# Optimization experiments

Measured on AMD Instinct MI355X. Metric: run time of the kernel, lower is better.

## Reference

```python
import jax, jax.numpy as jnp
import numpy as np

DIM = 64
N_GRAPHS = 300
N_NODES = 12000
N_EDGES = 40000


def setup_inputs() -> dict:
    key = jax.random.key(0)
    ks = jax.random.split(key, 16)
    N, E, F_IN, D = N_NODES, N_EDGES, 14, DIM

    def w(k, shape, fan_in):
        return jax.random.normal(k, shape, dtype=jnp.float32) / np.float32(np.sqrt(fan_in))

    return {
        "x": jax.random.normal(ks[0], (N, F_IN), dtype=jnp.float32),
        "edge_index": jax.random.randint(ks[1], (2, E), 0, N),
        "edge_attr": jax.random.uniform(ks[2], (E, 4), dtype=jnp.float32),
        "batch": jnp.sort(jax.random.randint(ks[3], (N,), 0, N_GRAPHS)),
        # lin0
        "lin0_w": w(ks[4], (D, F_IN), F_IN), "lin0_b": jnp.zeros((D,), jnp.float32),
        # edge MLP: Linear(4,128) -> ReLU -> Linear(128, D*D)
        "nn1_w": w(ks[5], (128, 4), 4), "nn1_b": jnp.zeros((128,), jnp.float32),
        "nn2_w": w(ks[6], (D * D, 128), 128), "nn2_b": jnp.zeros((D * D,), jnp.float32),
        # NNConv root weight + bias
        "root_w": w(ks[7], (D, D), D), "conv_b": jnp.zeros((D,), jnp.float32),
        # GRU(D, D), gate order r,z,n
        "gru_w_ih": w(ks[8], (3 * D, D), D), "gru_w_hh": w(ks[9], (3 * D, D), D),
        "gru_b_ih": jnp.zeros((3 * D,), jnp.float32), "gru_b_hh": jnp.zeros((3 * D,), jnp.float32),
        # Set2Set LSTM(2D -> D), gate order i,f,g,o
        "lstm_w_ih": w(ks[10], (4 * D, 2 * D), 2 * D), "lstm_w_hh": w(ks[11], (4 * D, D), D),
        "lstm_b_ih": jnp.zeros((4 * D,), jnp.float32), "lstm_b_hh": jnp.zeros((4 * D,), jnp.float32),
        # readout
        "lin1_w": w(ks[12], (D, 2 * D), 2 * D), "lin1_b": jnp.zeros((D,), jnp.float32),
        "lin2_w": w(ks[13], (1, D), D), "lin2_b": jnp.zeros((1,), jnp.float32),
    }


def _mpnn_forward(x, edge_index, edge_attr, batch,
                  lin0_w, lin0_b, nn1_w, nn1_b, nn2_w, nn2_b, root_w, conv_b,
                  gru_w_ih, gru_w_hh, gru_b_ih, gru_b_hh,
                  lstm_w_ih, lstm_w_hh, lstm_b_ih, lstm_b_hh,
                  lin1_w, lin1_b, lin2_w, lin2_b):
    N, D, B = x.shape[0], DIM, N_GRAPHS
    src, dst = edge_index[0], edge_index[1]

    out = jax.nn.relu(x @ lin0_w.T + lin0_b)          # [N, D]
    h = out

    # per-edge weight matrices from edge MLP: [E, D, D]
    W_e = (jax.nn.relu(edge_attr @ nn1_w.T + nn1_b) @ nn2_w.T + nn2_b).reshape(-1, D, D)
    deg = jnp.maximum(
        jax.ops.segment_sum(jnp.ones(src.shape, x.dtype), dst, num_segments=N), 1.0)

    for _ in range(3):
        # NNConv: gather -> per-edge bmm -> scatter-mean, plus root term and bias
        msg = jnp.einsum('ei,eio->eo', out[src], W_e)                 # [E, D]
        agg = jax.ops.segment_sum(msg, dst, num_segments=N) / deg[:, None]
        m = jax.nn.relu(out @ root_w + agg + conv_b)
        # GRU cell (torch gate order r, z, n)
        gx = m @ gru_w_ih.T + gru_b_ih
        gh = h @ gru_w_hh.T + gru_b_hh
        r = jax.nn.sigmoid(gx[:, :D] + gh[:, :D])
        z = jax.nn.sigmoid(gx[:, D:2 * D] + gh[:, D:2 * D])
        n = jnp.tanh(gx[:, 2 * D:] + r * gh[:, 2 * D:])
        h = (1.0 - z) * n + z * h
        out = h

    per_atom_out = out

    # Set2Set pooling, 3 processing steps
    q_star = jnp.zeros((B, 2 * D), x.dtype)
    hs = jnp.zeros((B, D), x.dtype)
    cs = jnp.zeros((B, D), x.dtype)
    for _ in range(3):
        gates = q_star @ lstm_w_ih.T + lstm_b_ih + hs @ lstm_w_hh.T + lstm_b_hh
        i_g = jax.nn.sigmoid(gates[:, 0 * D:1 * D])
        f_g = jax.nn.sigmoid(gates[:, 1 * D:2 * D])
        g_g = jnp.tanh(gates[:, 2 * D:3 * D])
        o_g = jax.nn.sigmoid(gates[:, 3 * D:4 * D])
        cs = f_g * cs + i_g * g_g
        hs = o_g * jnp.tanh(cs)
        q = hs                                                         # [B, D]
        e = jnp.sum(out * q[batch], axis=-1)                           # [N]
        e_max = jax.ops.segment_max(e, batch, num_segments=B)
        a = jnp.exp(e - e_max[batch])
        a = a / jax.ops.segment_sum(a, batch, num_segments=B)[batch]   # scatter-softmax
        r_read = jax.ops.segment_sum(a[:, None] * out, batch, num_segments=B)
        q_star = jnp.concatenate([q, r_read], axis=-1)                 # [B, 2D]

    y = jax.nn.relu(q_star @ lin1_w.T + lin1_b)
    y = (y @ lin2_w.T + lin2_b).reshape(-1)                            # [B]
    return (y, per_atom_out)


def reference(x, edge_index, edge_attr, batch,
              lin0_w, lin0_b, nn1_w, nn1_b, nn2_w, nn2_b, root_w, conv_b,
              gru_w_ih, gru_w_hh, gru_b_ih, gru_b_hh,
              lstm_w_ih, lstm_w_hh, lstm_b_ih, lstm_b_hh,
              lin1_w, lin1_b, lin2_w, lin2_b):
    return _mpnn_forward(x, edge_index, edge_attr, batch,
                         lin0_w, lin0_b, nn1_w, nn1_b, nn2_w, nn2_b, root_w, conv_b,
                         gru_w_ih, gru_w_hh, gru_b_ih, gru_b_hh,
                         lstm_w_ih, lstm_w_hh, lstm_b_ih, lstm_b_hh,
                         lin1_w, lin1_b, lin2_w, lin2_b)
```

## Files before the change

### kernel.cpp

```cpp
#include <hip/hip_runtime.h>
#include <math.h>

#define NBG 300
#define KP 8256

typedef __attribute__((ext_vector_type(8))) short short8_t;
typedef __attribute__((ext_vector_type(4))) float f32x4_t;

#define MFMA16(a,b,c) __builtin_amdgcn_mfma_f32_16x16x32_bf16(a,b,c,0,0,0)

__device__ __forceinline__ float sigmoidf_(float x){ return 1.0f/(1.0f+expf(-x)); }
__device__ __forceinline__ float bf2f(short s){
  union{unsigned u; float f;} v; v.u = ((unsigned)(unsigned short)s) << 16; return v.f;
}
__device__ __forceinline__ short f2bf(float f){
  union{float f; unsigned u;} v; v.f = f;
  unsigned r = (v.u + 0x7fffu + ((v.u >> 16) & 1u)) >> 16;
  return (short)r;
}
__device__ __forceinline__ unsigned cvt_pk_bf16(float lo, float hi){
  unsigned r;
  asm volatile("v_cvt_pk_bf16_f32 %0, %1, %2" : "=v"(r) : "v"(lo), "v"(hi));
  return r;
}
union FragA { short8_t v; unsigned u[4]; };

__device__ __forceinline__ short8_t frag_from(float sv, short8_t h){
  union { short8_t v; unsigned u[4]; } hh; hh.v = h;
  FragA fa;
  #pragma unroll
  for (int k2 = 0; k2 < 4; ++k2){
    float lo = __uint_as_float(hh.u[k2] << 16);
    float hi = __uint_as_float(hh.u[k2] & 0xffff0000u);
    fa.u[k2] = cvt_pk_bf16(sv*lo, sv*hi);
  }
  return fa.v;
}

__global__ void lin0_kernel(const float* __restrict__ x, const float* __restrict__ w,
                            const float* __restrict__ b, float* __restrict__ out,
                            short* __restrict__ out_bf, int N){
  int n = blockIdx.x; int d = threadIdx.x;
  __shared__ float xs[16];
  if (d < 14) xs[d] = x[n*14 + d];
  __syncthreads();
  float acc = b[d];
  #pragma unroll
  for (int k = 0; k < 14; ++k) acc = fmaf(xs[k], w[d*14 + k], acc);
  float v = fmaxf(acc, 0.0f);
  out[n*64 + d] = v;
  out_bf[n*64 + d] = f2bf(v);
}

__global__ void ehid_kernel(const float* __restrict__ ea, const float* __restrict__ w,
                            const float* __restrict__ b, short* __restrict__ hid_bf, int E){
  int e = blockIdx.x; int t = threadIdx.x;
  __shared__ float as[4];
  if (t < 4) as[t] = ea[e*4 + t];
  __syncthreads();
  float acc = b[t];
  #pragma unroll
  for (int k = 0; k < 4; ++k) acc = fmaf(as[k], w[t*4 + k], acc);
  hid_bf[(size_t)e*128 + t] = f2bf(fmaxf(acc, 0.0f));
}

__global__ void count2_kernel(const int* __restrict__ dstv, int E,
                              const int* __restrict__ batch, int N,
                              int* __restrict__ counts, int* __restrict__ bcounts){
  int i = blockIdx.x*blockDim.x + threadIdx.x;
  if (i < E) atomicAdd(&counts[dstv[i]], 1);
  int j = i - E;
  if (j >= 0 && j < N) atomicAdd(&bcounts[batch[j]], 1);
}

__global__ __launch_bounds__(1024) void scan2_kernel(
    const int* __restrict__ countsA, int* __restrict__ startsA, int* __restrict__ cursorA, int NA,
    const int* __restrict__ countsB, int* __restrict__ startsB, int* __restrict__ cursorB, int NB){
  const int* counts = blockIdx.x ? countsB : countsA;
  int* starts = blockIdx.x ? startsB : startsA;
  int* cursor = blockIdx.x ? cursorB : cursorA;
  int N = blockIdx.x ? NB : NA;
  __shared__ int part[1024];
  int t = threadIdx.x;
  int per = (N + 1023) >> 10;
  int base = t * per;
  int s = 0;
  for (int j = 0; j < per; ++j){ int idx = base + j; if (idx < N) s += counts[idx]; }
  part[t] = s;
  __syncthreads();
  for (int off = 1; off < 1024; off <<= 1){
    int v = (t >= off) ? part[t - off] : 0;
    __syncthreads();
    part[t] += v;
    __syncthreads();
  }
  int run = (t == 0) ? 0 : part[t-1];
  for (int j = 0; j < per; ++j){
    int idx = base + j;
    if (idx < N){ starts[idx] = run; cursor[idx] = run; run += counts[idx]; }
  }
}

__global__ void scatter_kernel(const int* __restrict__ dst, int* __restrict__ cursor,
                               int* __restrict__ sorted_eid, int E){
  int e = blockIdx.x*blockDim.x + threadIdx.x;
  if (e < E){ int p = atomicAdd(&cursor[dst[e]], 1); sorted_eid[p] = e; }
}

__global__ void w2t_build(const float* __restrict__ w2, const float* __restrict__ b2,
                          short* __restrict__ W2t){
  int o = blockIdx.x;
  for (int k = threadIdx.x; k < KP; k += blockDim.x){
    float val;
    if (k < 8192){ int i = k >> 7, h = k & 127; val = w2[(size_t)(i*64 + o)*128 + h]; }
    else val = b2[(k - 8192)*64 + o];
    W2t[(size_t)o*KP + k] = f2bf(val);
  }
}

__global__ __launch_bounds__(256) void msg_gemm3(
    const short* __restrict__ out_bf, const short* __restrict__ hid_bf,
    const short* __restrict__ W2t, const int* __restrict__ sorted,
    const int* __restrict__ src, const int* __restrict__ dstv,
    float* __restrict__ agg, int E)
{
  __shared__ short sSb[128*80];
  __shared__ __align__(16) char bufB[4][4096];
  __shared__ int eid_s[128];
  __shared__ int dst_s[128];

  const int tid = threadIdx.x;
  const int blk = blockIdx.x;
  const int split = blockIdx.y;

  if (tid < 128){
    int p = blk*128 + tid;
    int e = (p < E) ? sorted[p] : -1;
    eid_s[tid] = e;
    dst_s[tid] = (e >= 0) ? dstv[e] : -1;
  }
  __syncthreads();

  const int lane = tid & 63, wid = tid >> 6;
  const int r = lane & 15, q4 = lane >> 4;
  const int eloc0 = wid*32 + r;
  const int eloc1 = eloc0 + 16;

  short8_t z8 = {0,0,0,0,0,0,0,0};

  {
    int row = tid >> 1, half = tid & 1;
    int e = eid_s[row];
    short* dp = sSb + row*80 + half*32;
    if (e >= 0){
      const short* sp = out_bf + (size_t)src[e]*64 + half*32;
      *(short8_t*)(dp)      = *(const short8_t*)(sp);
      *(short8_t*)(dp + 8)  = *(const short8_t*)(sp + 8);
      *(short8_t*)(dp + 16) = *(const short8_t*)(sp + 16);
      *(short8_t*)(dp + 24) = *(const short8_t*)(sp + 24);
    } else {
      *(short8_t*)(dp) = z8; *(short8_t*)(dp + 8) = z8;
      *(short8_t*)(dp + 16) = z8; *(short8_t*)(dp + 24) = z8;
    }
  }

  short8_t hq0_0=z8, hq0_1=z8, hq0_2=z8, hq0_3=z8;
  short8_t hq1_0=z8, hq1_1=z8, hq1_2=z8, hq1_3=z8;
  {
    int e0 = eid_s[eloc0], e1 = eid_s[eloc1];
    if (e0 >= 0){
      const short* hp = hid_bf + (size_t)e0*128 + q4*8;
      hq0_0 = *(const short8_t*)(hp);      hq0_1 = *(const short8_t*)(hp + 32);
      hq0_2 = *(const short8_t*)(hp + 64); hq0_3 = *(const short8_t*)(hp + 96);
    }
    if (e1 >= 0){
      const short* hp = hid_bf + (size_t)e1*128 + q4*8;
      hq1_0 = *(const short8_t*)(hp);      hq1_1 = *(const short8_t*)(hp + 32);
      hq1_2 = *(const short8_t*)(hp + 64); hq1_3 = *(const short8_t*)(hp + 96);
    }
  }

  const int gl_o  = tid >> 2;
  const int gl_kq = (tid & 3) ^ ((tid >> 3) & 3);
  const char* w2b = (const char*)W2t;
  const size_t gbase = (size_t)gl_o*(KP*2) + (size_t)gl_kq*16;

  int boff0, boff1, boff2, boff3;
  {
    int o0 = r, o1 = 16 + r, o2 = 32 + r, o3 = 48 + r;
    boff0 = (o0*4 + (q4 ^ ((o0 >> 1) & 3))) * 16;
    boff1 = (o1*4 + (q4 ^ ((o1 >> 1) & 3))) * 16;
    boff2 = (o2*4 + (q4 ^ ((o2 >> 1) & 3))) * 16;
    boff3 = (o3*4 + (q4 ^ ((o3 >> 1) & 3))) * 16;
  }

  const bool last  = (split == 3);
  const int cstart = split * 64;
  const int nc     = last ? 66 : 64;
  const int clast  = cstart + nc - 1;

#define GLOAD(c_, bi_)                                                          \
  __builtin_amdgcn_global_load_lds(                                             \
      (const __attribute__((address_space(1))) unsigned*)(w2b + gbase + (size_t)(c_)*64), \
      (__attribute__((address_space(3))) unsigned*)(&bufB[bi_][wid*1024]), 16, 0, 0)

  GLOAD(cstart + 0, (cstart + 0) & 3);
  GLOAD(cstart + 1, (cstart + 1) & 3);
  GLOAD(cstart + 2, (cstart + 2) & 3);
  __syncthreads();

  f32x4_t zz = {0.f,0.f,0.f,0.f};
  f32x4_t acc00 = zz, acc01 = zz, acc02 = zz, acc03 = zz;
  f32x4_t acc10 = zz, acc11 = zz, acc12 = zz, acc13 = zz;

#define CHUNK(QI, Q, HQ0, HQ1)                                                  \
  {                                                                             \
    int c = cstart + (QI)*4 + (Q);                                              \
    asm volatile("s_waitcnt vmcnt(2) lgkmcnt(0)" ::: "memory");                 \
    __builtin_amdgcn_s_barrier();                                               \
    const char* bp = bufB[c & 3];                                               \
    short8_t b0 = *(const short8_t*)(bp + boff0);                               \
    short8_t b1 = *(const short8_t*)(bp + boff1);                               \
    short8_t b2 = *(const short8_t*)(bp + boff2);                               \
    short8_t b3 = *(const short8_t*)(bp + boff3);                               \
    { int cn = c + 3; if (cn > clast) cn = clast; GLOAD(cn, (c + 3) & 3); }     \
    short8_t f0 = frag_from(sv0, HQ0);                                          \
    short8_t f1 = frag_from(sv1, HQ1);                                          \
    acc00 = MFMA16(f0, b0, acc00);                                              \
    acc01 = MFMA16(f0, b1, acc01);                                              \
    acc02 = MFMA16(f0, b2, acc02);                                              \
    acc03 = MFMA16(f0, b3, acc03);                                              \
    acc10 = MFMA16(f1, b0, acc10);                                              \
    acc11 = MFMA16(f1, b1, acc11);                                              \
    acc12 = MFMA16(f1, b2, acc12);                                              \
    acc13 = MFMA16(f1, b3, acc13);                                              \
  }

  #pragma unroll 1
  for (int qi = 0; qi < 16; ++qi){
    int qg = (split << 4) + qi;
    float sv0 = bf2f(sSb[eloc0*80 + qg]);
    float sv1 = bf2f(sSb[eloc1*80 + qg]);
    CHUNK(qi, 0, hq0_0, hq1_0)
    CHUNK(qi, 1, hq0_1, hq1_1)
    CHUNK(qi, 2, hq0_2, hq1_2)
    CHUNK(qi, 3, hq0_3, hq1_3)
  }

  if (last){
    #pragma unroll 1
    for (int tc = 0; tc < 2; ++tc){
      int c = 256 + tc;
      asm volatile("s_waitcnt vmcnt(2) lgkmcnt(0)" ::: "memory");
      __builtin_amdgcn_s_barrier();
      const char* bp = bufB[c & 3];
      short8_t b0 = *(const short8_t*)(bp + boff0);
      short8_t b1 = *(const short8_t*)(bp + boff1);
      short8_t b2 = *(const short8_t*)(bp + boff2);
      short8_t b3 = *(const short8_t*)(bp + boff3);
      GLOAD(clast, (c + 3) & 3);
      short8_t f0 = *(const short8_t*)(sSb + eloc0*80 + tc*32 + q4*8);
      short8_t f1 = *(const short8_t*)(sSb + eloc1*80 + tc*32 + q4*8);
      acc00 = MFMA16(f0, b0, acc00);
      acc01 = MFMA16(f0, b1, acc01);
      acc02 = MFMA16(f0, b2, acc02);
      acc03 = MFMA16(f0, b3, acc03);
      acc10 = MFMA16(f1, b0, acc10);
      acc11 = MFMA16(f1, b1, acc11);
      acc12 = MFMA16(f1, b2, acc12);
      acc13 = MFMA16(f1, b3, acc13);
    }
  }

  asm volatile("s_waitcnt vmcnt(0)" ::: "memory");

  {
    int ebase = wid*32 + q4*4;
    float c0 = 0.f, c1 = 0.f, c2 = 0.f, c3 = 0.f;
    #pragma unroll
    for (int reg = 0; reg < 4; ++reg){
      c0 += acc00[reg]; c1 += acc01[reg]; c2 += acc02[reg]; c3 += acc03[reg];
      int d = dst_s[ebase + reg];
      int dn = (reg < 3) ? dst_s[ebase + reg + 1] : -2;
      if (d != dn){
        if (d >= 0){
          float* ap = agg + (size_t)d*64;
          atomicAdd(ap + r,      c0);
          atomicAdd(ap + 16 + r, c1);
          atomicAdd(ap + 32 + r, c2);
          atomicAdd(ap + 48 + r, c3);
        }
        c0 = c1 = c2 = c3 = 0.f;
      }
    }
  }
  {
    int ebase = wid*32 + 16 + q4*4;
    float c0 = 0.f, c1 = 0.f, c2 = 0.f, c3 = 0.f;
    #pragma unroll
    for (int reg = 0; reg < 4; ++reg){
      c0 += acc10[reg]; c1 += acc11[reg]; c2 += acc12[reg]; c3 += acc13[reg];
      int d = dst_s[ebase + reg];
      int dn = (reg < 3) ? dst_s[ebase + reg + 1] : -2;
      if (d != dn){
        if (d >= 0){
          float* ap = agg + (size_t)d*64;
          atomicAdd(ap + r,      c0);
          atomicAdd(ap + 16 + r, c1);
          atomicAdd(ap + 32 + r, c2);
          atomicAdd(ap + 48 + r, c3);
        }
        c0 = c1 = c2 = c3 = 0.f;
      }
    }
  }
#undef CHUNK
#undef GLOAD
}

__global__ __launch_bounds__(256) void node_mfma(
    const short* __restrict__ out_bf, float* __restrict__ agg,
    const int* __restrict__ counts,
    const float* __restrict__ root_w, const float* __restrict__ conv_b,
    const float* __restrict__ gwih, const float* __restrict__ gwhh,
    const float* __restrict__ gbih, const float* __restrict__ gbhh,
    float* __restrict__ out, short* __restrict__ out_bf_w,
    float* __restrict__ out_dup, int N)
{
  __shared__ short XH[64*128];
  __shared__ short rootT[64*64];
  __shared__ short Wih_s[192*64];
  __shared__ short Whh_s[192*64];
  __shared__ float rdeg_s[64];
  __shared__ float cb_s[64];

  int tid = threadIdx.x;
  int blk = blockIdx.x;
  int nbase = blk*64;

  {
    int n = tid >> 2, cq = tid & 3;
    int ng = nbase + n;
    short8_t v0 = {0,0,0,0,0,0,0,0}, v1 = v0;
    if (ng < N){
      const short* p = out_bf + (size_t)ng*64;
      v0 = *(const short8_t*)(p + cq*16);
      v1 = *(const short8_t*)(p + cq*16 + 8);
    }
    int c0 = 8 + cq*2;
    *(short8_t*)(XH + n*128 + ((c0     ^ (n & 7))*8)) = v0;
    *(short8_t*)(XH + n*128 + (((c0+1) ^ (n & 7))*8)) = v1;
  }
  {
    int i = tid >> 2, dq = tid & 3;
    #pragma unroll
    for (int j = 0; j < 16; ++j){
      int d = dq*16 + j;
      short v = f2bf(root_w[i*64 + d]);
      rootT[d*64 + (((i >> 3) ^ (d & 7))*8) + (i & 7)] = v;
    }
  }
  if (tid < 192){
    int g = tid;
    short pk[8];
    #pragma unroll
    for (int c = 0; c < 8; ++c){
      #pragma unroll
      for (int j = 0; j < 8; ++j) pk[j] = f2bf(gwih[g*64 + c*8 + j]);
      *(short8_t*)(Wih_s + g*64 + ((c ^ (g & 7))*8)) = *(short8_t*)&pk[0];
    }
    #pragma unroll
    for (int c = 0; c < 8; ++c){
      #pragma unroll
      for (int j = 0; j < 8; ++j) pk[j] = f2bf(gwhh[g*64 + c*8 + j]);
      *(short8_t*)(Whh_s + g*64 + ((c ^ (g & 7))*8)) = *(short8_t*)&pk[0];
    }
  }
  if (tid < 64){
    int ng = nbase + tid;
    int c = (ng < N) ? counts[ng] : 1;
    rdeg_s[tid] = 1.0f / fmaxf((float)c, 1.0f);
    cb_s[tid] = conv_b[tid];
  }
  __syncthreads();

  int lane = tid & 63, wid = tid >> 6;
  int r = lane & 15, q4 = lane >> 4;

  {
    int mh = (wid >> 1)*32, nh = (wid & 1)*32;
    f32x4_t z4 = {0.f,0.f,0.f,0.f};
    f32x4_t c00 = z4, c01 = z4, c10 = z4, c11 = z4;
    #pragma unroll
    for (int ks = 0; ks < 2; ++ks){
      int ck = 8 + ks*4 + q4;
      int swA = (ck ^ (r & 7))*8;
      int swB = ((ks*4 + q4) ^ (r & 7))*8;
      short8_t a0 = *(const short8_t*)(XH + (mh + r)*128 + swA);
      short8_t a1 = *(const short8_t*)(XH + (mh + 16 + r)*128 + swA);
      short8_t b0 = *(const short8_t*)(rootT + (nh + r)*64 + swB);
      short8_t b1 = *(const short8_t*)(rootT + (nh + 16 + r)*64 + swB);
      c00 = MFMA16(a0, b0, c00);
      c01 = MFMA16(a0, b1, c01);
      c10 = MFMA16(a1, b0, c10);
      c11 = MFMA16(a1, b1, c11);
    }
    #pragma unroll
    for (int mm = 0; mm < 2; ++mm){
      #pragma unroll
      for (int nn = 0; nn < 2; ++nn){
        f32x4_t cc = mm == 0 ? (nn == 0 ? c00 : c01) : (nn == 0 ? c10 : c11);
        int d = nh + nn*16 + r;
        #pragma unroll
        for (int reg = 0; reg < 4; ++reg){
          int n = mh + mm*16 + q4*4 + reg;
          int ng = nbase + n;
          float av = 0.0f;
          if (ng < N){
            av = agg[(size_t)ng*64 + d];
            agg[(size_t)ng*64 + d] = 0.0f;
          }
          float v = cc[reg] + av * rdeg_s[n] + cb_s[d];
          v = fmaxf(v, 0.0f);
          XH[n*128 + (((d >> 3) ^ (n & 7))*8) + (d & 7)] = f2bf(v);
        }
      }
    }
  }
  __syncthreads();

  f32x4_t ax[4][3], ah[4][3];
  {
    f32x4_t z4 = {0.f,0.f,0.f,0.f};
    #pragma unroll
    for (int mt = 0; mt < 4; ++mt)
      #pragma unroll
      for (int gt = 0; gt < 3; ++gt){ ax[mt][gt] = z4; ah[mt][gt] = z4; }
  }
  #pragma unroll
  for (int ks = 0; ks < 2; ++ks){
    int ckM = ks*4 + q4;
    int ckH = 8 + ks*4 + q4;
    int swM = (ckM ^ (r & 7))*8;
    int swH = (ckH ^ (r & 7))*8;
    int swB = ((ks*4 + q4) ^ (r & 7))*8;
    short8_t bx[3], bh[3];
    #pragma unroll
    for (int gt = 0; gt < 3; ++gt){
      int g = gt*64 + wid*16 + r;
      bx[gt] = *(const short8_t*)(Wih_s + g*64 + swB);
      bh[gt] = *(const short8_t*)(Whh_s + g*64 + swB);
    }
    #pragma unroll
    for (int mt = 0; mt < 4; ++mt){
      short8_t aM = *(const short8_t*)(XH + (mt*16 + r)*128 + swM);
      short8_t aH = *(const short8_t*)(XH + (mt*16 + r)*128 + swH);
      #pragma unroll
      for (int gt = 0; gt < 3; ++gt){
        ax[mt][gt] = MFMA16(aM, bx[gt], ax[mt][gt]);
        ah[mt][gt] = MFMA16(aH, bh[gt], ah[mt][gt]);
      }
    }
  }

  {
    int d = wid*16 + r;
    float bir = gbih[d],      bhr = gbhh[d];
    float biz = gbih[64 + d], bhz = gbhh[64 + d];
    float bin_ = gbih[128 + d], bhn = gbhh[128 + d];
    #pragma unroll
    for (int mt = 0; mt < 4; ++mt){
      #pragma unroll
      for (int reg = 0; reg < 4; ++reg){
        int n = mt*16 + q4*4 + reg;
        int ng = nbase + n;
        if (ng < N){
          float gxr = ax[mt][0][reg], gxz = ax[mt][1][reg], gxn = ax[mt][2][reg];
          float ghr = ah[mt][0][reg], ghz = ah[mt][1][reg], ghn = ah[mt][2][reg];
          float rr = sigmoidf_(gxr + ghr + bir + bhr);
          float zz = sigmoidf_(gxz + ghz + biz + bhz);
          float nn = tanhf(gxn + bin_ + rr*(ghn + bhn));
          float h = out[(size_t)ng*64 + d];
          float v = (1.0f - zz)*nn + zz*h;
          out[(size_t)ng*64 + d] = v;
          out_bf_w[(size_t)ng*64 + d] = f2bf(v);
          if (out_dup) out_dup[(size_t)ng*64 + d] = v;
        }
      }
    }
  }
}

__global__ __launch_bounds__(256) void set2set_kernel(
    const float* __restrict__ out, const int* __restrict__ bstarts,
    const int* __restrict__ bcounts,
    const float* __restrict__ lwih, const float* __restrict__ lwhh,
    const float* __restrict__ lbih, const float* __restrict__ lbhh,
    const float* __restrict__ l1w, const float* __restrict__ l1b,
    const float* __restrict__ l2w, const float* __restrict__ l2b,
    float* __restrict__ y)
{
  int b = blockIdx.x, t = threadIdx.x;
  int lane = t & 63, wid = t >> 6;
  __shared__ float qs[128];
  __shared__ float hsl[64], hs_s[64], cs_s[64];
  __shared__ float ev[512];
  __shared__ float red[256];
  __shared__ float rpart[4][64];
  __shared__ float scal[2];

  int s0 = bstarts[b], cnt = bcounts[b];
  if (cnt > 512) cnt = 512;
  if (t < 64){ hs_s[t] = 0.f; cs_s[t] = 0.f; }
  if (t < 128) qs[t] = 0.f;
  __syncthreads();

  for (int step = 0; step < 3; ++step){
    if (t < 64) hsl[t] = hs_s[t];
    __syncthreads();
    {
      float a0 = lbih[t] + lbhh[t], a1 = 0.f, a2 = 0.f, a3 = 0.f;
      const float* wi = lwih + t*128;
      #pragma unroll
      for (int kq = 0; kq < 32; ++kq){
        float4 w4 = *(const float4*)(wi + kq*4);
        a0 = fmaf(qs[kq*4+0], w4.x, a0);
        a1 = fmaf(qs[kq*4+1], w4.y, a1);
        a2 = fmaf(qs[kq*4+2], w4.z, a2);
        a3 = fmaf(qs[kq*4+3], w4.w, a3);
      }
      const float* wh = lwhh + t*64;
      #pragma unroll
      for (int kq = 0; kq < 16; ++kq){
        float4 w4 = *(const float4*)(wh + kq*4);
        a0 = fmaf(hsl[kq*4+0], w4.x, a0);
        a1 = fmaf(hsl[kq*4+1], w4.y, a1);
        a2 = fmaf(hsl[kq*4+2], w4.z, a2);
        a3 = fmaf(hsl[kq*4+3], w4.w, a3);
      }
      red[t] = (a0 + a1) + (a2 + a3);
    }
    __syncthreads();
    if (t < 64){
      float ig = sigmoidf_(red[t]);
      float fg = sigmoidf_(red[64 + t]);
      float gg = tanhf(red[128 + t]);
      float og = sigmoidf_(red[192 + t]);
      float c = fg*cs_s[t] + ig*gg;
      cs_s[t] = c;
      hs_s[t] = og*tanhf(c);
    }
    __syncthreads();

    float lmax = -1e30f;
    for (int idx = t; idx < cnt; idx += 256){
      const float* row = out + (size_t)(s0 + idx)*64;
      float a0 = 0.f, a1 = 0.f, a2 = 0.f, a3 = 0.f;
      #pragma unroll
      for (int kq = 0; kq < 16; ++kq){
        float4 v = *(const float4*)(row + kq*4);
        a0 = fmaf(v.x, hs_s[kq*4+0], a0);
        a1 = fmaf(v.y, hs_s[kq*4+1], a1);
        a2 = fmaf(v.z, hs_s[kq*4+2], a2);
        a3 = fmaf(v.w, hs_s[kq*4+3], a3);
      }
      float acc = (a0 + a1) + (a2 + a3);
      ev[idx] = acc;
      lmax = fmaxf(lmax, acc);
    }
    red[t] = lmax;
    __syncthreads();
    #pragma unroll
    for (int off = 128; off > 0; off >>= 1){
      if (t < off) red[t] = fmaxf(red[t], red[t + off]);
      __syncthreads();
    }
    if (t == 0) scal[0] = red[0];
    __syncthreads();
    float m = scal[0];

    float ls = 0.f;
    for (int idx = t; idx < cnt; idx += 256){
      float a = expf(ev[idx] - m);
      ev[idx] = a;
      ls += a;
    }
    red[t] = ls;
    __syncthreads();
    #pragma unroll
    for (int off = 128; off > 0; off >>= 1){
      if (t < off) red[t] += red[t + off];
      __syncthreads();
    }
    if (t == 0) scal[1] = red[0];
    __syncthreads();
    float lst = scal[1];

    float part = 0.f;
    for (int idx = wid; idx < cnt; idx += 4)
      part = fmaf(ev[idx], out[(size_t)(s0 + idx)*64 + lane], part);
    rpart[wid][lane] = part;
    __syncthreads();
    if (t < 64){
      float r = (rpart[0][t] + rpart[1][t]) + (rpart[2][t] + rpart[3][t]);
      r = (cnt > 0) ? r / lst : 0.f;
      qs[t] = hs_s[t];
      qs[64 + t] = r;
    }
    __syncthreads();
  }

  if (t < 64){
    float a0 = l1b[t], a1 = 0.f, a2 = 0.f, a3 = 0.f;
    const float* w1 = l1w + t*128;
    #pragma unroll
    for (int kq = 0; kq < 32; ++kq){
      float4 w4 = *(const float4*)(w1 + kq*4);
      a0 = fmaf(qs[kq*4+0], w4.x, a0);
      a1 = fmaf(qs[kq*4+1], w4.y, a1);
      a2 = fmaf(qs[kq*4+2], w4.z, a2);
      a3 = fmaf(qs[kq*4+3], w4.w, a3);
    }
    float acc = (a0 + a1) + (a2 + a3);
    float v = fmaxf(acc, 0.0f) * l2w[t];
    #pragma unroll
    for (int off = 32; off > 0; off >>= 1) v += __shfl_xor(v, off, 64);
    if (t == 0) y[b] = v + l2b[0];
  }
}

extern "C" void kernel_launch(void* const* d_in, const int* in_sizes, int n_in,
                              void* d_out, int out_size, void* d_ws, size_t ws_size,
                              hipStream_t stream){
  const float* x      = (const float*)d_in[0];
  const int*   ei     = (const int*)  d_in[1];
  const float* ea     = (const float*)d_in[2];
  const int*   batch  = (const int*)  d_in[3];
  const float* lin0_w = (const float*)d_in[4];
  const float* lin0_b = (const float*)d_in[5];
  const float* nn1_w  = (const float*)d_in[6];
  const float* nn1_b  = (const float*)d_in[7];
  const float* nn2_w  = (const float*)d_in[8];
  const float* nn2_b  = (const float*)d_in[9];
  const float* root_w = (const float*)d_in[10];
  const float* conv_b = (const float*)d_in[11];
  const float* gwih   = (const float*)d_in[12];
  const float* gwhh   = (const float*)d_in[13];
  const float* gbih   = (const float*)d_in[14];
  const float* gbhh   = (const float*)d_in[15];
  const float* lwih   = (const float*)d_in[16];
  const float* lwhh   = (const float*)d_in[17];
  const float* lbih   = (const float*)d_in[18];
  const float* lbhh   = (const float*)d_in[19];
  const float* l1w    = (const float*)d_in[20];
  const float* l1b    = (const float*)d_in[21];
  const float* l2w    = (const float*)d_in[22];
  const float* l2b    = (const float*)d_in[23];

  const int N = in_sizes[0] / 14;
  const int E = in_sizes[1] / 2;
  const int B = NBG;
  const int* src  = ei;
  const int* dstv = ei + E;

  char* wsp = (char*)d_ws; size_t off = 0;
  auto alloc = [&](size_t bytes)->char* {
    char* p = wsp + off; off += (bytes + 255) & ~((size_t)255); return p;
  };
  float* out     = (float*)alloc((size_t)N*64*4);
  short* out_bf  = (short*)alloc((size_t)N*64*2);
  float* agg     = (float*)alloc((size_t)N*64*4);
  int*   counts  = (int*)  alloc((size_t)N*4);
  int*   bcounts = (int*)  alloc((size_t)B*4);
  int*   starts  = (int*)  alloc((size_t)N*4);
  int*   cursor  = (int*)  alloc((size_t)N*4);
  int*   sorted  = (int*)  alloc((size_t)E*4);
  int*   bstarts = (int*)  alloc((size_t)B*4);
  int*   bcursor = (int*)  alloc((size_t)B*4);
  short* hid_bf  = (short*)alloc((size_t)E*128*2);
  short* W2t     = (short*)alloc((size_t)64*KP*2);

  lin0_kernel<<<N, 64, 0, stream>>>(x, lin0_w, lin0_b, out, out_bf, N);
  ehid_kernel<<<E, 128, 0, stream>>>(ea, nn1_w, nn1_b, hid_bf, E);

  size_t cspan = (((size_t)N*4 + 255) & ~(size_t)255) + (size_t)B*4;
  hipMemsetAsync(counts, 0, cspan, stream);
  count2_kernel<<<(E + N + 255)/256, 256, 0, stream>>>(dstv, E, batch, N, counts, bcounts);
  scan2_kernel<<<2, 1024, 0, stream>>>(counts, starts, cursor, N,
                                       bcounts, bstarts, bcursor, B);
  scatter_kernel<<<(E + 255)/256, 256, 0, stream>>>(dstv, cursor, sorted, E);

  w2t_build<<<64, 256, 0, stream>>>(nn2_w, nn2_b, W2t);
  hipMemsetAsync(agg, 0, (size_t)N*64*4, stream);

  int mblocks = (E + 127)/128;
  int nblocks = (N + 63)/64;
  dim3 mg(mblocks, 4);
  for (int it = 0; it < 3; ++it){
    msg_gemm3<<<mg, 256, 0, stream>>>(out_bf, hid_bf, W2t, sorted, src, dstv, agg, E);
    node_mfma<<<nblocks, 256, 0, stream>>>(out_bf, agg, counts, root_w, conv_b,
                                           gwih, gwhh, gbih, gbhh, out, out_bf,
                                           (it == 2) ? ((float*)d_out + 300) : nullptr, N);
  }

  set2set_kernel<<<B, 256, 0, stream>>>(out, bstarts, bcounts, lwih, lwhh, lbih, lbhh,
                                        l1w, l1b, l2w, l2b, (float*)d_out);
}
```

Measured before the change: 353.0 us.

## Halve message GEMM block to two waves, each computing 64 edges per wave

The per-edge message GEMM block shrinks from 4 waves to 2 waves (128 threads) while keeping 128 edges per block. Each wave now handles four 16-edge M tiles instead of two, so every B fragment read from LDS feeds twice as many MFMAs. Each thread issues two async global-to-LDS loads per chunk to fill the W2t buffer, with the wait count adjusted to match. The cost is doubled accumulator and hidden-fragment register pressure and fewer waves per block to hide latency.

```diff
diff --git a/kernel.cpp b/kernel.cpp
--- a/kernel.cpp
+++ b/kernel.cpp
@@ -118,7 +118,7 @@
   }
 }
 
-__global__ __launch_bounds__(256) void msg_gemm3(
+__global__ __launch_bounds__(128) void msg_gemm5(
     const short* __restrict__ out_bf, const short* __restrict__ hid_bf,
     const short* __restrict__ W2t, const int* __restrict__ sorted,
     const int* __restrict__ src, const int* __restrict__ dstv,
@@ -133,7 +133,7 @@
   const int blk = blockIdx.x;
   const int split = blockIdx.y;
 
-  if (tid < 128){
+  {
     int p = blk*128 + tid;
     int e = (p < E) ? sorted[p] : -1;
     eid_s[tid] = e;
@@ -143,31 +143,38 @@
 
   const int lane = tid & 63, wid = tid >> 6;
   const int r = lane & 15, q4 = lane >> 4;
-  const int eloc0 = wid*32 + r;
-  const int eloc1 = eloc0 + 16;
+  const int el0 = wid*64 + r;
+  const int el1 = el0 + 16;
+  const int el2 = el0 + 32;
+  const int el3 = el0 + 48;
 
   short8_t z8 = {0,0,0,0,0,0,0,0};
 
   {
-    int row = tid >> 1, half = tid & 1;
-    int e = eid_s[row];
-    short* dp = sSb + row*80 + half*32;
+    int e = eid_s[tid];
+    short* dp = sSb + tid*80;
     if (e >= 0){
-      const short* sp = out_bf + (size_t)src[e]*64 + half*32;
+      const short* sp = out_bf + (size_t)src[e]*64;
       *(short8_t*)(dp)      = *(const short8_t*)(sp);
       *(short8_t*)(dp + 8)  = *(const short8_t*)(sp + 8);
       *(short8_t*)(dp + 16) = *(const short8_t*)(sp + 16);
       *(short8_t*)(dp + 24) = *(const short8_t*)(sp + 24);
+      *(short8_t*)(dp + 32) = *(const short8_t*)(sp + 32);
+      *(short8_t*)(dp + 40) = *(const short8_t*)(sp + 40);
+      *(short8_t*)(dp + 48) = *(const short8_t*)(sp + 48);
+      *(short8_t*)(dp + 56) = *(const short8_t*)(sp + 56);
     } else {
-      *(short8_t*)(dp) = z8; *(short8_t*)(dp + 8) = z8;
-      *(short8_t*)(dp + 16) = z8; *(short8_t*)(dp + 24) = z8;
+      #pragma unroll
+      for (int j = 0; j < 8; ++j) *(short8_t*)(dp + j*8) = z8;
     }
   }
 
   short8_t hq0_0=z8, hq0_1=z8, hq0_2=z8, hq0_3=z8;
   short8_t hq1_0=z8, hq1_1=z8, hq1_2=z8, hq1_3=z8;
-  {
-    int e0 = eid_s[eloc0], e1 = eid_s[eloc1];
+  short8_t hq2_0=z8, hq2_1=z8, hq2_2=z8, hq2_3=z8;
+  short8_t hq3_0=z8, hq3_1=z8, hq3_2=z8, hq3_3=z8;
+  {
+    int e0 = eid_s[el0], e1 = eid_s[el1], e2 = eid_s[el2], e3 = eid_s[el3];
     if (e0 >= 0){
       const short* hp = hid_bf + (size_t)e0*128 + q4*8;
       hq0_0 = *(const short8_t*)(hp);      hq0_1 = *(const short8_t*)(hp + 32);
@@ -178,12 +185,23 @@
       hq1_0 = *(const short8_t*)(hp);      hq1_1 = *(const short8_t*)(hp + 32);
       hq1_2 = *(const short8_t*)(hp + 64); hq1_3 = *(const short8_t*)(hp + 96);
     }
+    if (e2 >= 0){
+      const short* hp = hid_bf + (size_t)e2*128 + q4*8;
+      hq2_0 = *(const short8_t*)(hp);      hq2_1 = *(const short8_t*)(hp + 32);
+      hq2_2 = *(const short8_t*)(hp + 64); hq2_3 = *(const short8_t*)(hp + 96);
+    }
+    if (e3 >= 0){
+      const short* hp = hid_bf + (size_t)e3*128 + q4*8;
+      hq3_0 = *(const short8_t*)(hp);      hq3_1 = *(const short8_t*)(hp + 32);
+      hq3_2 = *(const short8_t*)(hp + 64); hq3_3 = *(const short8_t*)(hp + 96);
+    }
   }
 
   const int gl_o  = tid >> 2;
   const int gl_kq = (tid & 3) ^ ((tid >> 3) & 3);
   const char* w2b = (const char*)W2t;
-  const size_t gbase = (size_t)gl_o*(KP*2) + (size_t)gl_kq*16;
+  const size_t gbase  = (size_t)gl_o*(KP*2) + (size_t)gl_kq*16;
+  const size_t gbase2 = gbase + (size_t)32*(KP*2);
 
   int boff0, boff1, boff2, boff3;
   {
@@ -199,123 +217,122 @@
   const int nc     = last ? 66 : 64;
   const int clast  = cstart + nc - 1;
 
-#define GLOAD(c_, bi_)                                                          \
-  __builtin_amdgcn_global_load_lds(                                             \
-      (const __attribute__((address_space(1))) unsigned*)(w2b + gbase + (size_t)(c_)*64), \
-      (__attribute__((address_space(3))) unsigned*)(&bufB[bi_][wid*1024]), 16, 0, 0)
-
-  GLOAD(cstart + 0, (cstart + 0) & 3);
-  GLOAD(cstart + 1, (cstart + 1) & 3);
-  GLOAD(cstart + 2, (cstart + 2) & 3);
+#define GLOAD2(c_, bi_)                                                         \
+  do {                                                                          \
+    __builtin_amdgcn_global_load_lds(                                           \
+        (const __attribute__((address_space(1))) unsigned*)(w2b + gbase + (size_t)(c_)*64),  \
+        (__attribute__((address_space(3))) unsigned*)(&bufB[bi_][wid*1024]), 16, 0, 0);      \
+    __builtin_amdgcn_global_load_lds(                                           \
+        (const __attribute__((address_space(1))) unsigned*)(w2b + gbase2 + (size_t)(c_)*64), \
+        (__attribute__((address_space(3))) unsigned*)(&bufB[bi_][2048 + wid*1024]), 16, 0, 0); \
+  } while (0)
+
+  GLOAD2(cstart + 0, (cstart + 0) & 3);
+  GLOAD2(cstart + 1, (cstart + 1) & 3);
+  GLOAD2(cstart + 2, (cstart + 2) & 3);
   __syncthreads();
 
   f32x4_t zz = {0.f,0.f,0.f,0.f};
-  f32x4_t acc00 = zz, acc01 = zz, acc02 = zz, acc03 = zz;
-  f32x4_t acc10 = zz, acc11 = zz, acc12 = zz, acc13 = zz;
-
-#define CHUNK(QI, Q, HQ0, HQ1)                                                  \
+  f32x4_t a00 = zz, a01 = zz, a02 = zz, a03 = zz;
+  f32x4_t a10 = zz, a11 = zz, a12 = zz, a13 = zz;
+  f32x4_t a20 = zz, a21 = zz, a22 = zz, a23 = zz;
+  f32x4_t a30 = zz, a31 = zz, a32 = zz, a33 = zz;
+
+#define CHUNK(QI, Q, H0, H1, H2, H3)                                            \
   {                                                                             \
     int c = cstart + (QI)*4 + (Q);                                              \
-    asm volatile("s_waitcnt vmcnt(2) lgkmcnt(0)" ::: "memory");                 \
+    asm volatile("s_waitcnt vmcnt(4) lgkmcnt(0)" ::: "memory");                 \
     __builtin_amdgcn_s_barrier();                                               \
     const char* bp = bufB[c & 3];                                               \
     short8_t b0 = *(const short8_t*)(bp + boff0);                               \
     short8_t b1 = *(const short8_t*)(bp + boff1);                               \
     short8_t b2 = *(const short8_t*)(bp + boff2);                               \
     short8_t b3 = *(const short8_t*)(bp + boff3);                               \
-    { int cn = c + 3; if (cn > clast) cn = clast; GLOAD(cn, (c + 3) & 3); }     \
-    short8_t f0 = frag_from(sv0, HQ0);                                          \
-    short8_t f1 = frag_from(sv1, HQ1);                                          \
-    acc00 = MFMA16(f0, b0, acc00);                                              \
-    acc01 = MFMA16(f0, b1, acc01);                                              \
-    acc02 = MFMA16(f0, b2, acc02);                                              \
-    acc03 = MFMA16(f0, b3, acc03);                                              \
-    acc10 = MFMA16(f1, b0, acc10);                                              \
-    acc11 = MFMA16(f1, b1, acc11);                                              \
-    acc12 = MFMA16(f1, b2, acc12);                                              \
-    acc13 = MFMA16(f1, b3, acc13);                                              \
+    { int cn = c + 3; if (cn > clast) cn = clast; GLOAD2(cn, (c + 3) & 3); }    \
+    short8_t f0 = frag_from(sv0, H0);                                           \
+    a00 = MFMA16(f0, b0, a00); a01 = MFMA16(f0, b1, a01);                       \
+    a02 = MFMA16(f0, b2, a02); a03 = MFMA16(f0, b3, a03);                       \
+    short8_t f1 = frag_from(sv1, H1);                                           \
+    a10 = MFMA16(f1, b0, a10); a11 = MFMA16(f1, b1, a11);                       \
+    a12 = MFMA16(f1, b2, a12); a13 = MFMA16(f1, b3, a13);                       \
+    short8_t f2 = frag_from(sv2, H2);                                           \
+    a20 = MFMA16(f2, b0, a20); a21 = MFMA16(f2, b1, a21);                       \
+    a22 = MFMA16(f2, b2, a22); a23 = MFMA16(f2, b3, a23);                       \
+    short8_t f3 = frag_from(sv3, H3);                                           \
+    a30 = MFMA16(f3, b0, a30); a31 = MFMA16(f3, b1, a31);                       \
+    a32 = MFMA16(f3, b2, a32); a33 = MFMA16(f3, b3, a33);                       \
   }
 
   #pragma unroll 1
   for (int qi = 0; qi < 16; ++qi){
     int qg = (split << 4) + qi;
-    float sv0 = bf2f(sSb[eloc0*80 + qg]);
-    float sv1 = bf2f(sSb[eloc1*80 + qg]);
-    CHUNK(qi, 0, hq0_0, hq1_0)
-    CHUNK(qi, 1, hq0_1, hq1_1)
-    CHUNK(qi, 2, hq0_2, hq1_2)
-    CHUNK(qi, 3, hq0_3, hq1_3)
+    float sv0 = bf2f(sSb[el0*80 + qg]);
+    float sv1 = bf2f(sSb[el1*80 + qg]);
+    float sv2 = bf2f(sSb[el2*80 + qg]);
+    float sv3 = bf2f(sSb[el3*80 + qg]);
+    CHUNK(qi, 0, hq0_0, hq1_0, hq2_0, hq3_0)
+    CHUNK(qi, 1, hq0_1, hq1_1, hq2_1, hq3_1)
+    CHUNK(qi, 2, hq0_2, hq1_2, hq2_2, hq3_2)
+    CHUNK(qi, 3, hq0_3, hq1_3, hq2_3, hq3_3)
   }
 
   if (last){
     #pragma unroll 1
     for (int tc = 0; tc < 2; ++tc){
       int c = 256 + tc;
-      asm volatile("s_waitcnt vmcnt(2) lgkmcnt(0)" ::: "memory");
+      asm volatile("s_waitcnt vmcnt(4) lgkmcnt(0)" ::: "memory");
       __builtin_amdgcn_s_barrier();
       const char* bp = bufB[c & 3];
       short8_t b0 = *(const short8_t*)(bp + boff0);
       short8_t b1 = *(const short8_t*)(bp + boff1);
       short8_t b2 = *(const short8_t*)(bp + boff2);
       short8_t b3 = *(const short8_t*)(bp + boff3);
-      GLOAD(clast, (c + 3) & 3);
-      short8_t f0 = *(const short8_t*)(sSb + eloc0*80 + tc*32 + q4*8);
-      short8_t f1 = *(const short8_t*)(sSb + eloc1*80 + tc*32 + q4*8);
-      acc00 = MFMA16(f0, b0, acc00);
-      acc01 = MFMA16(f0, b1, acc01);
-      acc02 = MFMA16(f0, b2, acc02);
-      acc03 = MFMA16(f0, b3, acc03);
-      acc10 = MFMA16(f1, b0, acc10);
-      acc11 = MFMA16(f1, b1, acc11);
-      acc12 = MFMA16(f1, b2, acc12);
-      acc13 = MFMA16(f1, b3, acc13);
+      GLOAD2(clast, (c + 3) & 3);
+      short8_t f0 = *(const short8_t*)(sSb + el0*80 + tc*32 + q4*8);
+      short8_t f1 = *(const short8_t*)(sSb + el1*80 + tc*32 + q4*8);
+      short8_t f2 = *(const short8_t*)(sSb + el2*80 + tc*32 + q4*8);
+      short8_t f3 = *(const short8_t*)(sSb + el3*80 + tc*32 + q4*8);
+      a00 = MFMA16(f0, b0, a00); a01 = MFMA16(f0, b1, a01);
+      a02 = MFMA16(f0, b2, a02); a03 = MFMA16(f0, b3, a03);
+      a10 = MFMA16(f1, b0, a10); a11 = MFMA16(f1, b1, a11);
+      a12 = MFMA16(f1, b2, a12); a13 = MFMA16(f1, b3, a13);
+      a20 = MFMA16(f2, b0, a20); a21 = MFMA16(f2, b1, a21);
+      a22 = MFMA16(f2, b2, a22); a23 = MFMA16(f2, b3, a23);
+      a30 = MFMA16(f3, b0, a30); a31 = MFMA16(f3, b1, a31);
+      a32 = MFMA16(f3, b2, a32); a33 = MFMA16(f3, b3, a33);
     }
   }
 
   asm volatile("s_waitcnt vmcnt(0)" ::: "memory");
 
-  {
-    int ebase = wid*32 + q4*4;
-    float c0 = 0.f, c1 = 0.f, c2 = 0.f, c3 = 0.f;
-    #pragma unroll
-    for (int reg = 0; reg < 4; ++reg){
-      c0 += acc00[reg]; c1 += acc01[reg]; c2 += acc02[reg]; c3 += acc03[reg];
-      int d = dst_s[ebase + reg];
-      int dn = (reg < 3) ? dst_s[ebase + reg + 1] : -2;
-      if (d != dn){
-        if (d >= 0){
-          float* ap = agg + (size_t)d*64;
-          atomicAdd(ap + r,      c0);
-          atomicAdd(ap + 16 + r, c1);
-          atomicAdd(ap + 32 + r, c2);
-          atomicAdd(ap + 48 + r, c3);
-        }
-        c0 = c1 = c2 = c3 = 0.f;
-      }
-    }
-  }
-  {
-    int ebase = wid*32 + 16 + q4*4;
-    float c0 = 0.f, c1 = 0.f, c2 = 0.f, c3 = 0.f;
-    #pragma unroll
-    for (int reg = 0; reg < 4; ++reg){
-      c0 += acc10[reg]; c1 += acc11[reg]; c2 += acc12[reg]; c3 += acc13[reg];
-      int d = dst_s[ebase + reg];
-      int dn = (reg < 3) ? dst_s[ebase + reg + 1] : -2;
-      if (d != dn){
-        if (d >= 0){
-          float* ap = agg + (size_t)d*64;
-          atomicAdd(ap + r,      c0);
-          atomicAdd(ap + 16 + r, c1);
-          atomicAdd(ap + 32 + r, c2);
-          atomicAdd(ap + 48 + r, c3);
-        }
-        c0 = c1 = c2 = c3 = 0.f;
-      }
-    }
-  }
+#define SCAT(MT, A0, A1, A2, A3)                                                \
+  {                                                                             \
+    int ebase = wid*64 + (MT)*16 + q4*4;                                        \
+    float c0 = 0.f, c1 = 0.f, c2 = 0.f, c3 = 0.f;                               \
+    _Pragma("unroll")                                                           \
+    for (int reg = 0; reg < 4; ++reg){                                          \
+      c0 += A0[reg]; c1 += A1[reg]; c2 += A2[reg]; c3 += A3[reg];               \
+      int d = dst_s[ebase + reg];                                               \
+      int dn = (reg < 3) ? dst_s[ebase + reg + 1] : -2;                         \
+      if (d != dn){                                                             \
+        if (d >= 0){                                                            \
+          float* ap = agg + (size_t)d*64;                                       \
+          atomicAdd(ap + r,      c0);                                           \
+          atomicAdd(ap + 16 + r, c1);                                           \
+          atomicAdd(ap + 32 + r, c2);                                           \
+          atomicAdd(ap + 48 + r, c3);                                           \
+        }                                                                       \
+        c0 = c1 = c2 = c3 = 0.f;                                                \
+      }                                                                         \
+    }                                                                           \
+  }
+  SCAT(0, a00, a01, a02, a03)
+  SCAT(1, a10, a11, a12, a13)
+  SCAT(2, a20, a21, a22, a23)
+  SCAT(3, a30, a31, a32, a33)
+#undef SCAT
 #undef CHUNK
-#undef GLOAD
+#undef GLOAD2
 }
 
 __global__ __launch_bounds__(256) void node_mfma(
@@ -697,7 +714,7 @@
   int nblocks = (N + 63)/64;
   dim3 mg(mblocks, 4);
   for (int it = 0; it < 3; ++it){
-    msg_gemm3<<<mg, 256, 0, stream>>>(out_bf, hid_bf, W2t, sorted, src, dstv, agg, E);
+    msg_gemm5<<<mg, 128, 0, stream>>>(out_bf, hid_bf, W2t, sorted, src, dstv, agg, E);
     node_mfma<<<nblocks, 256, 0, stream>>>(out_bf, agg, counts, root_w, conv_b,
                                            gwih, gwhh, gbih, gbhh, out, out_bf,
                                            (it == 2) ? ((float*)d_out + 300) : nullptr, N);
```

After: 443.6 us. 1.26x slower.

## Load W2 fragments directly into registers instead of LDS ring buffer

Applied to the files above, without the earlier changes.

The message GEMM no longer stages W2t chunks through a 4-deep LDS ring filled with global_load_lds. Each lane now reads its B fragments straight from global memory into registers, software-pipelined four chunks ahead. This removes the per-chunk block barrier and the LDS round trip, and frees 16KB of shared memory. In exchange every wave fetches the full weight tile itself instead of sharing it, so L2 traffic and register pressure go up.

```diff
diff --git a/kernel.cpp b/kernel.cpp
--- a/kernel.cpp
+++ b/kernel.cpp
@@ -118,14 +118,13 @@
   }
 }
 
-__global__ __launch_bounds__(256) void msg_gemm3(
+__global__ __launch_bounds__(256) void msg_gemm7(
     const short* __restrict__ out_bf, const short* __restrict__ hid_bf,
     const short* __restrict__ W2t, const int* __restrict__ sorted,
     const int* __restrict__ src, const int* __restrict__ dstv,
     float* __restrict__ agg, int E)
 {
   __shared__ short sSb[128*80];
-  __shared__ __align__(16) char bufB[4][4096];
   __shared__ int eid_s[128];
   __shared__ int dst_s[128];
 
@@ -180,60 +179,48 @@
     }
   }
 
-  const int gl_o  = tid >> 2;
-  const int gl_kq = (tid & 3) ^ ((tid >> 3) & 3);
-  const char* w2b = (const char*)W2t;
-  const size_t gbase = (size_t)gl_o*(KP*2) + (size_t)gl_kq*16;
-
-  int boff0, boff1, boff2, boff3;
-  {
-    int o0 = r, o1 = 16 + r, o2 = 32 + r, o3 = 48 + r;
-    boff0 = (o0*4 + (q4 ^ ((o0 >> 1) & 3))) * 16;
-    boff1 = (o1*4 + (q4 ^ ((o1 >> 1) & 3))) * 16;
-    boff2 = (o2*4 + (q4 ^ ((o2 >> 1) & 3))) * 16;
-    boff3 = (o3*4 + (q4 ^ ((o3 >> 1) & 3))) * 16;
-  }
-
-  const bool last  = (split == 3);
+  const short* w2p0 = W2t + (size_t)(r)      *KP + q4*8;
+  const short* w2p1 = W2t + (size_t)(16 + r) *KP + q4*8;
+  const short* w2p2 = W2t + (size_t)(32 + r) *KP + q4*8;
+  const short* w2p3 = W2t + (size_t)(48 + r) *KP + q4*8;
+
+#define BLOAD(P, c_)                                                            \
+  do { size_t kb = (size_t)(c_)*32;                                             \
+    P##_0 = *(const short8_t*)(w2p0 + kb);                                      \
+    P##_1 = *(const short8_t*)(w2p1 + kb);                                      \
+    P##_2 = *(const short8_t*)(w2p2 + kb);                                      \
+    P##_3 = *(const short8_t*)(w2p3 + kb); } while (0)
+
   const int cstart = split * 64;
-  const int nc     = last ? 66 : 64;
-  const int clast  = cstart + nc - 1;
-
-#define GLOAD(c_, bi_)                                                          \
-  __builtin_amdgcn_global_load_lds(                                             \
-      (const __attribute__((address_space(1))) unsigned*)(w2b + gbase + (size_t)(c_)*64), \
-      (__attribute__((address_space(3))) unsigned*)(&bufB[bi_][wid*1024]), 16, 0, 0)
-
-  GLOAD(cstart + 0, (cstart + 0) & 3);
-  GLOAD(cstart + 1, (cstart + 1) & 3);
-  GLOAD(cstart + 2, (cstart + 2) & 3);
+
+  short8_t B0_0=z8,B0_1=z8,B0_2=z8,B0_3=z8;
+  short8_t B1_0=z8,B1_1=z8,B1_2=z8,B1_3=z8;
+  short8_t B2_0=z8,B2_1=z8,B2_2=z8,B2_3=z8;
+  short8_t B3_0=z8,B3_1=z8,B3_2=z8,B3_3=z8;
+  BLOAD(B0, cstart + 0);
+  BLOAD(B1, cstart + 1);
+  BLOAD(B2, cstart + 2);
+  BLOAD(B3, cstart + 3);
+
   __syncthreads();
 
   f32x4_t zz = {0.f,0.f,0.f,0.f};
-  f32x4_t acc00 = zz, acc01 = zz, acc02 = zz, acc03 = zz;
-  f32x4_t acc10 = zz, acc11 = zz, acc12 = zz, acc13 = zz;
-
-#define CHUNK(QI, Q, HQ0, HQ1)                                                  \
+  f32x4_t acc0 = zz, acc1 = zz, acc2 = zz, acc3 = zz;
+  f32x4_t acc4 = zz, acc5 = zz, acc6 = zz, acc7 = zz;
+
+#define QSTEP(P, H0, H1, QI, Q)                                                 \
   {                                                                             \
-    int c = cstart + (QI)*4 + (Q);                                              \
-    asm volatile("s_waitcnt vmcnt(2) lgkmcnt(0)" ::: "memory");                 \
-    __builtin_amdgcn_s_barrier();                                               \
-    const char* bp = bufB[c & 3];                                               \
-    short8_t b0 = *(const short8_t*)(bp + boff0);                               \
-    short8_t b1 = *(const short8_t*)(bp + boff1);                               \
-    short8_t b2 = *(const short8_t*)(bp + boff2);                               \
-    short8_t b3 = *(const short8_t*)(bp + boff3);                               \
-    { int cn = c + 3; if (cn > clast) cn = clast; GLOAD(cn, (c + 3) & 3); }     \
-    short8_t f0 = frag_from(sv0, HQ0);                                          \
-    short8_t f1 = frag_from(sv1, HQ1);                                          \
-    acc00 = MFMA16(f0, b0, acc00);                                              \
-    acc01 = MFMA16(f0, b1, acc01);                                              \
-    acc02 = MFMA16(f0, b2, acc02);                                              \
-    acc03 = MFMA16(f0, b3, acc03);                                              \
-    acc10 = MFMA16(f1, b0, acc10);                                              \
-    acc11 = MFMA16(f1, b1, acc11);                                              \
-    acc12 = MFMA16(f1, b2, acc12);                                              \
-    acc13 = MFMA16(f1, b3, acc13);                                              \
+    short8_t f0 = frag_from(sv0, H0);                                           \
+    short8_t f1 = frag_from(sv1, H1);                                           \
+    acc0 = MFMA16(f0, P##_0, acc0);                                             \
+    acc1 = MFMA16(f0, P##_1, acc1);                                             \
+    acc2 = MFMA16(f0, P##_2, acc2);                                             \
+    acc3 = MFMA16(f0, P##_3, acc3);                                             \
+    acc4 = MFMA16(f1, P##_0, acc4);                                             \
+    acc5 = MFMA16(f1, P##_1, acc5);                                             \
+    acc6 = MFMA16(f1, P##_2, acc6);                                             \
+    acc7 = MFMA16(f1, P##_3, acc7);                                             \
+    if ((QI) < 15) BLOAD(P, cstart + ((QI)+1)*4 + (Q));                         \
   }
 
   #pragma unroll 1
@@ -241,45 +228,47 @@
     int qg = (split << 4) + qi;
     float sv0 = bf2f(sSb[eloc0*80 + qg]);
     float sv1 = bf2f(sSb[eloc1*80 + qg]);
-    CHUNK(qi, 0, hq0_0, hq1_0)
-    CHUNK(qi, 1, hq0_1, hq1_1)
-    CHUNK(qi, 2, hq0_2, hq1_2)
-    CHUNK(qi, 3, hq0_3, hq1_3)
-  }
-
-  if (last){
-    #pragma unroll 1
+    QSTEP(B0, hq0_0, hq1_0, qi, 0)
+    QSTEP(B1, hq0_1, hq1_1, qi, 1)
+    QSTEP(B2, hq0_2, hq1_2, qi, 2)
+    QSTEP(B3, hq0_3, hq1_3, qi, 3)
+  }
+
+  if (split == 3){
+    BLOAD(B0, 256);
+    BLOAD(B1, 257);
+    #pragma unroll
     for (int tc = 0; tc < 2; ++tc){
-      int c = 256 + tc;
-      asm volatile("s_waitcnt vmcnt(2) lgkmcnt(0)" ::: "memory");
-      __builtin_amdgcn_s_barrier();
-      const char* bp = bufB[c & 3];
-      short8_t b0 = *(const short8_t*)(bp + boff0);
-      short8_t b1 = *(const short8_t*)(bp + boff1);
-      short8_t b2 = *(const short8_t*)(bp + boff2);
-      short8_t b3 = *(const short8_t*)(bp + boff3);
-      GLOAD(clast, (c + 3) & 3);
       short8_t f0 = *(const short8_t*)(sSb + eloc0*80 + tc*32 + q4*8);
       short8_t f1 = *(const short8_t*)(sSb + eloc1*80 + tc*32 + q4*8);
-      acc00 = MFMA16(f0, b0, acc00);
-      acc01 = MFMA16(f0, b1, acc01);
-      acc02 = MFMA16(f0, b2, acc02);
-      acc03 = MFMA16(f0, b3, acc03);
-      acc10 = MFMA16(f1, b0, acc10);
-      acc11 = MFMA16(f1, b1, acc11);
-      acc12 = MFMA16(f1, b2, acc12);
-      acc13 = MFMA16(f1, b3, acc13);
-    }
-  }
-
-  asm volatile("s_waitcnt vmcnt(0)" ::: "memory");
+      if (tc == 0){
+        acc0 = MFMA16(f0, B0_0, acc0);
+        acc1 = MFMA16(f0, B0_1, acc1);
+        acc2 = MFMA16(f0, B0_2, acc2);
+        acc3 = MFMA16(f0, B0_3, acc3);
+        acc4 = MFMA16(f1, B0_0, acc4);
+        acc5 = MFMA16(f1, B0_1, acc5);
+        acc6 = MFMA16(f1, B0_2, acc6);
+        acc7 = MFMA16(f1, B0_3, acc7);
+      } else {
+        acc0 = MFMA16(f0, B1_0, acc0);
+        acc1 = MFMA16(f0, B1_1, acc1);
+        acc2 = MFMA16(f0, B1_2, acc2);
+        acc3 = MFMA16(f0, B1_3, acc3);
+        acc4 = MFMA16(f1, B1_0, acc4);
+        acc5 = MFMA16(f1, B1_1, acc5);
+        acc6 = MFMA16(f1, B1_2, acc6);
+        acc7 = MFMA16(f1, B1_3, acc7);
+      }
+    }
+  }
 
   {
     int ebase = wid*32 + q4*4;
     float c0 = 0.f, c1 = 0.f, c2 = 0.f, c3 = 0.f;
     #pragma unroll
     for (int reg = 0; reg < 4; ++reg){
-      c0 += acc00[reg]; c1 += acc01[reg]; c2 += acc02[reg]; c3 += acc03[reg];
+      c0 += acc0[reg]; c1 += acc1[reg]; c2 += acc2[reg]; c3 += acc3[reg];
       int d = dst_s[ebase + reg];
       int dn = (reg < 3) ? dst_s[ebase + reg + 1] : -2;
       if (d != dn){
@@ -299,7 +288,7 @@
     float c0 = 0.f, c1 = 0.f, c2 = 0.f, c3 = 0.f;
     #pragma unroll
     for (int reg = 0; reg < 4; ++reg){
-      c0 += acc10[reg]; c1 += acc11[reg]; c2 += acc12[reg]; c3 += acc13[reg];
+      c0 += acc4[reg]; c1 += acc5[reg]; c2 += acc6[reg]; c3 += acc7[reg];
       int d = dst_s[ebase + reg];
       int dn = (reg < 3) ? dst_s[ebase + reg + 1] : -2;
       if (d != dn){
@@ -314,8 +303,8 @@
       }
     }
   }
-#undef CHUNK
-#undef GLOAD
+#undef QSTEP
+#undef BLOAD
 }
 
 __global__ __launch_bounds__(256) void node_mfma(
@@ -697,7 +686,7 @@
   int nblocks = (N + 63)/64;
   dim3 mg(mblocks, 4);
   for (int it = 0; it < 3; ++it){
-    msg_gemm3<<<mg, 256, 0, stream>>>(out_bf, hid_bf, W2t, sorted, src, dstv, agg, E);
+    msg_gemm7<<<mg, 256, 0, stream>>>(out_bf, hid_bf, W2t, sorted, src, dstv, agg, E);
     node_mfma<<<nblocks, 256, 0, stream>>>(out_bf, agg, counts, root_w, conv_b,
                                            gwih, gwhh, gbih, gbhh, out, out_bf,
                                            (it == 2) ? ((float*)d_out + 300) : nullptr, N);
```

After: 645.3 us. 82.8% more time.
